# Kernel tuning notes

Hardware: AMD Instinct MI355X
Metric: run time of the kernel (lower is better)

Reference implementation:

```python
import jax, jax.numpy as jnp
import numpy as np

MOMENTUM = 0.1  # from init_kwargs


def setup_inputs() -> dict:
    key = jax.random.key(0)
    k1, k2 = jax.random.split(key)
    # [B, C, H, W] image batch
    x = jax.random.normal(k1, (32, 3, 512, 512), dtype=jnp.float32)
    # running amplitude buffer [C, H, W]; nonzero -> EMA branch is exercised
    running_amp = jax.random.uniform(k2, (3, 512, 512), dtype=jnp.float32)
    return {"x": x, "running_amp": running_amp}


def reference(x, running_amp):
    # FFT over spatial dims
    fft = jnp.fft.fft2(x, axes=(-2, -1))                     # [B,C,H,W] complex64
    amp = jnp.fft.fftshift(jnp.abs(fft), axes=(-2, -1))      # centered amplitude
    pha = jnp.angle(fft)                                     # phase

    # EMA update of running amplitude (batch-mean); if buffer is all-zero it is
    # initialized to the batch mean (mirrors the torch `sum == 0` branch).
    amp_mean = jnp.mean(amp, axis=0)                         # [C,H,W]
    new_amp = jnp.where(
        jnp.sum(running_amp) == 0,
        amp_mean,
        (1.0 - MOMENTUM) * running_amp + MOMENTUM * amp_mean,
    )

    # substitute amplitude with the (updated) running amplitude, keep phase
    amp_sub = jnp.fft.ifftshift(new_amp, axes=(-2, -1))      # [C,H,W]
    out = jnp.real(jnp.fft.ifft2(amp_sub * jnp.exp(1j * pha), axes=(-2, -1)))
    return out.astype(x.dtype)
```

## Files before the change

### kernel.cpp

```cpp
#include <hip/hip_runtime.h>
#include <math.h>

#define NB 32
#define NC 3
#define HH 512
#define WW 512
#define W2 272


__device__ __forceinline__ int swz(int i){ int h=(i>>6)&7; return i ^ (h<<3) ^ h; }
__device__ __forceinline__ int rev9(int k){ return ((k&7)<<6) | (k&56) | (k>>6); }

__device__ __forceinline__ float sin2pi(float x){
#if __has_builtin(__builtin_amdgcn_sinf)
  return __builtin_amdgcn_sinf(x);
#else
  return __sinf(6.28318530717958647692f*x);
#endif
}
__device__ __forceinline__ float cos2pi(float x){
#if __has_builtin(__builtin_amdgcn_cosf)
  return __builtin_amdgcn_cosf(x);
#else
  return __cosf(6.28318530717958647692f*x);
#endif
}

template<int S>
__device__ __forceinline__ void dft8(float* xr, float* xi){
  const float r2 = 0.70710678118654752f;
  float tr[4], ti[4], mr[4], mi[4];
#pragma unroll
  for(int n=0;n<4;n++){
    tr[n]=xr[n]+xr[n+4]; ti[n]=xi[n]+xi[n+4];
    mr[n]=xr[n]-xr[n+4]; mi[n]=xi[n]-xi[n+4];
  }
  float or_[4], oi_[4];
  or_[0]=mr[0];               oi_[0]=mi[0];
  or_[1]=r2*(mr[1]-S*mi[1]);  oi_[1]=r2*(mi[1]+S*mr[1]);
  or_[2]=-S*mi[2];            oi_[2]= S*mr[2];
  or_[3]=-r2*(mr[3]+S*mi[3]); oi_[3]= r2*(S*mr[3]-mi[3]);
  float s0r=tr[0]+tr[2], s0i=ti[0]+ti[2];
  float s1r=tr[1]+tr[3], s1i=ti[1]+ti[3];
  float d0r=tr[0]-tr[2], d0i=ti[0]-ti[2];
  float d1r=tr[1]-tr[3], d1i=ti[1]-ti[3];
  xr[0]=s0r+s1r;   xi[0]=s0i+s1i;
  xr[4]=s0r-s1r;   xi[4]=s0i-s1i;
  xr[2]=d0r-S*d1i; xi[2]=d0i+S*d1r;
  xr[6]=d0r+S*d1i; xi[6]=d0i-S*d1r;
  float p0r=or_[0]+or_[2], p0i=oi_[0]+oi_[2];
  float p1r=or_[1]+or_[3], p1i=oi_[1]+oi_[3];
  float e0r=or_[0]-or_[2], e0i=oi_[0]-oi_[2];
  float e1r=or_[1]-or_[3], e1i=oi_[1]-oi_[3];
  xr[1]=p0r+p1r;   xi[1]=p0i+p1i;
  xr[5]=p0r-p1r;   xi[5]=p0i-p1i;
  xr[3]=e0r-S*e1i; xi[3]=e0i+S*e1r;
  xr[7]=e0r+S*e1i; xi[7]=e0i-S*e1r;
}

template<int S>
__device__ __forceinline__ void twid(float* xr, float* xi, int n, float invM){
  float f = (float)n * invM;
  float c1 = cos2pi(f), s1 = (float)S * sin2pi(f);
  float cr=c1, ci=s1;
#pragma unroll
  for(int q=1;q<8;q++){
    float a=xr[q], b=xi[q];
    xr[q]=a*cr-b*ci; xi[q]=a*ci+b*cr;
    float nr=cr*c1-ci*s1, ni=cr*s1+ci*c1;
    cr=nr; ci=ni;
  }
}

__global__ __launch_bounds__(256) void k_row_rfft(const float* __restrict__ x, float2* __restrict__ Fh,
                                                  int c0, unsigned long long fh_cs){
  __shared__ float lre[4][512];
  __shared__ float lim[4][512];
  const int wv = threadIdx.x>>6, t = threadIdx.x&63;
  const int pr = blockIdx.x*4 + wv;
  const int b = pr>>8, r2 = pr&255;
  const int cc = blockIdx.y, c = c0 + cc;
  const float* sa = x + (size_t)b*(NC*HH*WW) + (size_t)c*HH*WW + (size_t)(2*r2)*WW;
  const float* sb = sa + WW;
  float xr[8], xi[8];
#pragma unroll
  for(int i=0;i<8;i++){ xr[i]=sa[t+64*i]; xi[i]=sb[t+64*i]; }
  dft8<-1>(xr,xi);
  twid<-1>(xr,xi,t,1.0f/512.0f);
#pragma unroll
  for(int q=0;q<8;q++){ int p=swz(t+64*q); lre[wv][p]=xr[q]; lim[wv][p]=xi[q]; }
  __syncthreads();
  const int beta=t>>3, n1=t&7, base1=64*beta+n1;
#pragma unroll
  for(int i=0;i<8;i++){ int p=swz(base1+8*i); xr[i]=lre[wv][p]; xi[i]=lim[wv][p]; }
  dft8<-1>(xr,xi);
  twid<-1>(xr,xi,n1,1.0f/64.0f);
#pragma unroll
  for(int q=0;q<8;q++){ int p=swz(base1+8*q); lre[wv][p]=xr[q]; lim[wv][p]=xi[q]; }
  __syncthreads();
#pragma unroll
  for(int i=0;i<8;i++){ int p=swz(8*t+i); xr[i]=lre[wv][p]; xi[i]=lim[wv][p]; }
  dft8<-1>(xr,xi);
  __syncthreads();
#pragma unroll
  for(int i=0;i<8;i++){ int nat = 64*i + 8*(t&7) + (t>>3); lre[wv][nat]=xr[i]; lim[wv][nat]=xi[i]; }
  __syncthreads();
  float2* Fa = Fh + (size_t)cc*fh_cs + (size_t)(b*HH + 2*r2)*W2;
  float2* Fb = Fa + W2;
#pragma unroll
  for(int j=0;j<5;j++){
    int w = t + 64*j;
    if(w<=256){
      int m = (512-w)&511;
      float pr_=lre[wv][w], pi_=lim[wv][w], qr=lre[wv][m], qi=lim[wv][m];
      Fa[w]=make_float2(0.5f*(pr_+qr), 0.5f*(pi_-qi));
      Fb[w]=make_float2(0.5f*(pi_+qi), 0.5f*(qr-pr_));
    }
  }
}

__global__ __launch_bounds__(512) void k_col_fft(float2* __restrict__ Fh, unsigned long long fh_cs){
  __shared__ float sre[512*17];
  __shared__ float sim[512*17];
  const int b    = blockIdx.x/17;
  const int tile = blockIdx.x - b*17;
  const int w0   = tile*16;
  float2* base = Fh + (size_t)blockIdx.y*fh_cs + (size_t)b*HH*W2 + w0;
  const int c = threadIdx.x&15, w = threadIdx.x>>4;
#pragma unroll
  for(int k=0;k<16;k++){
    int f = threadIdx.x + 512*k;
    int r = f>>4, col = f&15;
    float2 v = base[(size_t)r*W2 + col];
    sre[r*17+col]=v.x; sim[r*17+col]=v.y;
  }
  __syncthreads();
#pragma unroll
  for(int jj=0;jj<2;jj++){
    int n = jj*32 + w;
    float xr[8], xi[8];
#pragma unroll
    for(int i=0;i<8;i++){ int e=n+64*i; xr[i]=sre[e*17+c]; xi[i]=sim[e*17+c]; }
    dft8<-1>(xr,xi);
    twid<-1>(xr,xi,n,1.0f/512.0f);
#pragma unroll
    for(int q=0;q<8;q++){ int e=n+64*q; sre[e*17+c]=xr[q]; sim[e*17+c]=xi[q]; }
  }
  __syncthreads();
#pragma unroll
  for(int jj=0;jj<2;jj++){
    int m = jj*32 + w;
    int bb = m>>3, nn = m&7, bs = 64*bb+nn;
    float xr[8], xi[8];
#pragma unroll
    for(int i=0;i<8;i++){ int e=bs+8*i; xr[i]=sre[e*17+c]; xi[i]=sim[e*17+c]; }
    dft8<-1>(xr,xi);
    twid<-1>(xr,xi,nn,1.0f/64.0f);
#pragma unroll
    for(int q=0;q<8;q++){ int e=bs+8*q; sre[e*17+c]=xr[q]; sim[e*17+c]=xi[q]; }
  }
  __syncthreads();
#pragma unroll
  for(int jj=0;jj<2;jj++){
    int m = jj*32+w;
    float xr[8], xi[8];
#pragma unroll
    for(int i=0;i<8;i++){ int e=8*m+i; xr[i]=sre[e*17+c]; xi[i]=sim[e*17+c]; }
    dft8<-1>(xr,xi);
#pragma unroll
    for(int q=0;q<8;q++){ int e=8*m+q; sre[e*17+c]=xr[q]; sim[e*17+c]=xi[q]; }
  }
  __syncthreads();
#pragma unroll
  for(int k=0;k<16;k++){
    int f=threadIdx.x+512*k;
    int r=f>>4, col=f&15;
    if(w0+col<=256)
      base[(size_t)r*W2+col]=make_float2(sre[r*17+col], sim[r*17+col]);
  }
}

__global__ __launch_bounds__(256) void k_rsum(const float* __restrict__ ra, float* __restrict__ out, int n){
  float s=0.f;
  for(int i=blockIdx.x*256+threadIdx.x; i<n; i+=gridDim.x*256) s+=ra[i];
#pragma unroll
  for(int off=32;off>=1;off>>=1) s += __shfl_down(s, off, 64);
  if((threadIdx.x&63)==0) atomicAdd(out, s);
}

__global__ __launch_bounds__(256) void k_amp(const float2* __restrict__ Fh, unsigned long long fh_cs,
                                             const float* __restrict__ ra, const float* __restrict__ rsum,
                                             float* __restrict__ A, unsigned long long a_cs, int c0){
  int f = blockIdx.x*256 + threadIdx.x;
  int p = f/W2, w = f - p*W2;
  if(w>256) return;
  const int cc = blockIdx.y, c = c0 + cc;
  const float2* Fc = Fh + (size_t)cc*fh_cs;
  const float* rac = ra + (size_t)c*HH*WW;
  float s=0.f;
#pragma unroll 8
  for(int b=0;b<NB;b++){
    float2 v = Fc[((size_t)b*HH + p)*W2 + w];
    s += sqrtf(v.x*v.x+v.y*v.y);
  }
  float mean = s*(1.0f/32.0f);
  int h = rev9(p);
  int hs =(h+256)&511, ws =(w+256)&511;
  int hs2=(256-h)&511, ws2=(256-w)&511;
  float a_ = (rsum[0]==0.0f) ? mean
           : 0.45f*(rac[hs*WW+ws] + rac[hs2*WW+ws2]) + 0.1f*mean;
  A[(size_t)cc*a_cs + f]=a_;
}

__global__ __launch_bounds__(512) void k_col_ifft(float2* __restrict__ Fh, unsigned long long fh_cs,
                                                  const float* __restrict__ A, unsigned long long a_cs){
  __shared__ float sre[512*17];
  __shared__ float sim[512*17];
  const int b    = blockIdx.x/17;
  const int tile = blockIdx.x - b*17;
  const int w0   = tile*16;
  float2* base = Fh + (size_t)blockIdx.y*fh_cs + (size_t)b*HH*W2 + w0;
  const float* Aa = A + (size_t)blockIdx.y*a_cs + w0;
  const int c = threadIdx.x&15, w = threadIdx.x>>4;
  const float invN2 = 1.0f/262144.0f;
#pragma unroll
  for(int k=0;k<16;k++){
    int f=threadIdx.x+512*k;
    int r=f>>4, col=f&15;
    float2 v = base[(size_t)r*W2+col];
    float amp = Aa[(size_t)r*W2+col];
    float mag = sqrtf(v.x*v.x + v.y*v.y);
    float fr, fi;
    if(mag > 0.f){ float sc = amp*invN2/mag; fr=v.x*sc; fi=v.y*sc; }
    else         { fr = amp*invN2; fi=0.f; }
    sre[r*17+col]=fr; sim[r*17+col]=fi;
  }
  __syncthreads();
#pragma unroll
  for(int jj=0;jj<2;jj++){
    int m = jj*32+w;
    float xr[8], xi[8];
#pragma unroll
    for(int q=0;q<8;q++){ int e=8*m+q; xr[q]=sre[e*17+c]; xi[q]=sim[e*17+c]; }
    dft8<1>(xr,xi);
#pragma unroll
    for(int i=0;i<8;i++){ int e=8*m+i; sre[e*17+c]=xr[i]; sim[e*17+c]=xi[i]; }
  }
  __syncthreads();
#pragma unroll
  for(int jj=0;jj<2;jj++){
    int m = jj*32 + w;
    int bb = m>>3, nn = m&7, bs = 64*bb+nn;
    float xr[8], xi[8];
#pragma unroll
    for(int q=0;q<8;q++){ int e=bs+8*q; xr[q]=sre[e*17+c]; xi[q]=sim[e*17+c]; }
    twid<1>(xr,xi,nn,1.0f/64.0f);
    dft8<1>(xr,xi);
#pragma unroll
    for(int i=0;i<8;i++){ int e=bs+8*i; sre[e*17+c]=xr[i]; sim[e*17+c]=xi[i]; }
  }
  __syncthreads();
#pragma unroll
  for(int jj=0;jj<2;jj++){
    int n = jj*32+w;
    float xr[8], xi[8];
#pragma unroll
    for(int q=0;q<8;q++){ int e=n+64*q; xr[q]=sre[e*17+c]; xi[q]=sim[e*17+c]; }
    twid<1>(xr,xi,n,1.0f/512.0f);
    dft8<1>(xr,xi);
#pragma unroll
    for(int i=0;i<8;i++){ int e=n+64*i; sre[e*17+c]=xr[i]; sim[e*17+c]=xi[i]; }
  }
  __syncthreads();
#pragma unroll
  for(int k=0;k<16;k++){
    int f=threadIdx.x+512*k;
    int r=f>>4, col=f&15;
    if(w0+col<=256)
      base[(size_t)r*W2+col]=make_float2(sre[r*17+col], sim[r*17+col]);
  }
}

__global__ __launch_bounds__(256) void k_row_irfft(const float2* __restrict__ Fh, unsigned long long fh_cs,
                                                   float* __restrict__ out, int c0){
  __shared__ float gAr[4][264], gAi[4][264], gBr[4][264], gBi[4][264];
  __shared__ float lre[4][512], lim[4][512];
  const int wv=threadIdx.x>>6, t=threadIdx.x&63;
  const int pr = blockIdx.x*4+wv;
  const int b = pr>>8, r2 = pr&255;
  const int cc = blockIdx.y, c = c0 + cc;
  const float2* Rp = Fh + (size_t)cc*fh_cs + (size_t)(b*HH + 2*r2)*W2;
  const float2* Rq = Rp + W2;
#pragma unroll
  for(int j=0;j<5;j++){
    int w = t + 64*j;
    if(w<=256){
      float2 v = Rp[w]; gAr[wv][w]=v.x; gAi[wv][w]=v.y;
      float2 u = Rq[w]; gBr[wv][w]=u.x; gBi[wv][w]=u.y;
    }
  }
  __syncthreads();
  float xr[8], xi[8];
#pragma unroll
  for(int i=0;i<8;i++){
    int w = rev9(8*t+i);
    float zr, zi;
    if(w<=256){ zr = gAr[wv][w]-gBi[wv][w]; zi = gAi[wv][w]+gBr[wv][w]; }
    else{
      int m = 512-w;
      zr = gAr[wv][m]+gBi[wv][m]; zi = gBr[wv][m]-gAi[wv][m];
    }
    xr[i]=zr; xi[i]=zi;
  }
  dft8<1>(xr,xi);
#pragma unroll
  for(int i=0;i<8;i++){ int pp=swz(8*t+i); lre[wv][pp]=xr[i]; lim[wv][pp]=xi[i]; }
  __syncthreads();
  const int beta=t>>3, n1=t&7, base1=64*beta+n1;
#pragma unroll
  for(int qq=0;qq<8;qq++){ int pp=swz(base1+8*qq); xr[qq]=lre[wv][pp]; xi[qq]=lim[wv][pp]; }
  twid<1>(xr,xi,n1,1.0f/64.0f);
  dft8<1>(xr,xi);
#pragma unroll
  for(int i=0;i<8;i++){ int pp=swz(base1+8*i); lre[wv][pp]=xr[i]; lim[wv][pp]=xi[i]; }
  __syncthreads();
#pragma unroll
  for(int qq=0;qq<8;qq++){ int pp=swz(t+64*qq); xr[qq]=lre[wv][pp]; xi[qq]=lim[wv][pp]; }
  twid<1>(xr,xi,t,1.0f/512.0f);
  dft8<1>(xr,xi);
  float* oa = out + (size_t)b*(NC*HH*WW) + (size_t)c*HH*WW + (size_t)(2*r2)*WW;
  float* ob = oa + WW;
#pragma unroll
  for(int i=0;i<8;i++){ oa[t+64*i]=xr[i]; ob[t+64*i]=xi[i]; }
}

extern "C" void kernel_launch(void* const* d_in, const int* in_sizes, int n_in,
                              void* d_out, int out_size, void* d_ws, size_t ws_size,
                              hipStream_t stream) {
  const float* x  = (const float*)d_in[0];
  const float* ra = (const float*)d_in[1];
  float* out = (float*)d_out;

  const unsigned long long fh_cs = (unsigned long long)NB*HH*W2;
  const unsigned long long a_cs  = (unsigned long long)HH*W2;
  const size_t fb1 = (size_t)fh_cs*sizeof(float2);
  const size_t ab1 = (size_t)a_cs*sizeof(float);
  const size_t need3 = 3*fb1 + 3*ab1 + 64;
  const size_t need1 = fb1 + ab1 + 64;

  if (ws_size >= need3) {
    float2* Fh   = (float2*)d_ws;
    float*  A    = (float*)((char*)d_ws + 3*fb1);
    float*  rsum = (float*)((char*)A + 3*ab1);
    hipMemsetAsync(rsum, 0, sizeof(float), stream);
    k_rsum<<<768,256,0,stream>>>(ra, rsum, NC*HH*WW);
    k_row_rfft <<<dim3(NB*256/4,3), 256, 0, stream>>>(x, Fh, 0, fh_cs);
    k_col_fft  <<<dim3(NB*17,3),    512, 0, stream>>>(Fh, fh_cs);
    k_amp      <<<dim3(HH*W2/256,3),256, 0, stream>>>(Fh, fh_cs, ra, rsum, A, a_cs, 0);
    k_col_ifft <<<dim3(NB*17,3),    512, 0, stream>>>(Fh, fh_cs, A, a_cs);
    k_row_irfft<<<dim3(NB*256/4,3), 256, 0, stream>>>(Fh, fh_cs, out, 0);
  } else if (ws_size >= need1) {
    float2* Fh   = (float2*)d_ws;
    float*  A    = (float*)((char*)d_ws + fb1);
    float*  rsum = (float*)((char*)A + ab1);
    hipMemsetAsync(rsum, 0, sizeof(float), stream);
    k_rsum<<<768,256,0,stream>>>(ra, rsum, NC*HH*WW);
    for(int c=0;c<NC;c++){
      k_row_rfft <<<dim3(NB*256/4,1), 256, 0, stream>>>(x, Fh, c, 0ULL);
      k_col_fft  <<<dim3(NB*17,1),    512, 0, stream>>>(Fh, 0ULL);
      k_amp      <<<dim3(HH*W2/256,1),256, 0, stream>>>(Fh, 0ULL, ra, rsum, A, 0ULL, c);
      k_col_ifft <<<dim3(NB*17,1),    512, 0, stream>>>(Fh, 0ULL, A, 0ULL);
      k_row_irfft<<<dim3(NB*256/4,1), 256, 0, stream>>>(Fh, 0ULL, out, c);
    }
  }
}
```

Baseline: 241.6 us.

## Fuse amplitude batch-sum into column FFT and load/store columns directly from global

The column FFT and inverse FFT kernels now read the first stage and write the last stage directly from and to global memory, skipping the shared-memory staging passes and their barriers. The column FFT also accumulates per-frequency magnitudes into a zeroed buffer with atomicAdd, so the amplitude kernel no longer rereads the whole spectrum across the batch and only finalizes the mean and EMA. The per-channel fallback path for small workspaces is removed, and the inverse uses rsqrt instead of sqrt and a divide. The trade-offs are strided, less coalesced global accesses and 32-way atomic contention per output element.

```diff
diff --git a/kernel.cpp b/kernel.cpp
--- a/kernel.cpp
+++ b/kernel.cpp
@@ -73,14 +73,14 @@
 }
 
 __global__ __launch_bounds__(256) void k_row_rfft(const float* __restrict__ x, float2* __restrict__ Fh,
-                                                  int c0, unsigned long long fh_cs){
+                                                  unsigned long long fh_cs){
   __shared__ float lre[4][512];
   __shared__ float lim[4][512];
   const int wv = threadIdx.x>>6, t = threadIdx.x&63;
   const int pr = blockIdx.x*4 + wv;
   const int b = pr>>8, r2 = pr&255;
-  const int cc = blockIdx.y, c = c0 + cc;
-  const float* sa = x + (size_t)b*(NC*HH*WW) + (size_t)c*HH*WW + (size_t)(2*r2)*WW;
+  const int cc = blockIdx.y;
+  const float* sa = x + (size_t)b*(NC*HH*WW) + (size_t)cc*HH*WW + (size_t)(2*r2)*WW;
   const float* sb = sa + WW;
   float xr[8], xi[8];
 #pragma unroll
@@ -119,28 +119,23 @@
   }
 }
 
-__global__ __launch_bounds__(512) void k_col_fft(float2* __restrict__ Fh, unsigned long long fh_cs){
+__global__ __launch_bounds__(512) void k_col_fft(float2* __restrict__ Fh, unsigned long long fh_cs,
+                                                 float* __restrict__ Asum, unsigned long long a_cs){
   __shared__ float sre[512*17];
   __shared__ float sim[512*17];
   const int b    = blockIdx.x/17;
   const int tile = blockIdx.x - b*17;
   const int w0   = tile*16;
-  float2* base = Fh + (size_t)blockIdx.y*fh_cs + (size_t)b*HH*W2 + w0;
+  const int cc   = blockIdx.y;
+  float2* base = Fh + (size_t)cc*fh_cs + (size_t)b*HH*W2 + w0;
+  float*  As   = Asum + (size_t)cc*a_cs + w0;
   const int c = threadIdx.x&15, w = threadIdx.x>>4;
 #pragma unroll
-  for(int k=0;k<16;k++){
-    int f = threadIdx.x + 512*k;
-    int r = f>>4, col = f&15;
-    float2 v = base[(size_t)r*W2 + col];
-    sre[r*17+col]=v.x; sim[r*17+col]=v.y;
-  }
-  __syncthreads();
-#pragma unroll
   for(int jj=0;jj<2;jj++){
     int n = jj*32 + w;
     float xr[8], xi[8];
 #pragma unroll
-    for(int i=0;i<8;i++){ int e=n+64*i; xr[i]=sre[e*17+c]; xi[i]=sim[e*17+c]; }
+    for(int i=0;i<8;i++){ float2 v = base[(size_t)(n+64*i)*W2 + c]; xr[i]=v.x; xi[i]=v.y; }
     dft8<-1>(xr,xi);
     twid<-1>(xr,xi,n,1.0f/512.0f);
 #pragma unroll
@@ -167,16 +162,14 @@
 #pragma unroll
     for(int i=0;i<8;i++){ int e=8*m+i; xr[i]=sre[e*17+c]; xi[i]=sim[e*17+c]; }
     dft8<-1>(xr,xi);
-#pragma unroll
-    for(int q=0;q<8;q++){ int e=8*m+q; sre[e*17+c]=xr[q]; sim[e*17+c]=xi[q]; }
-  }
-  __syncthreads();
-#pragma unroll
-  for(int k=0;k<16;k++){
-    int f=threadIdx.x+512*k;
-    int r=f>>4, col=f&15;
-    if(w0+col<=256)
-      base[(size_t)r*W2+col]=make_float2(sre[r*17+col], sim[r*17+col]);
+    if(w0+c<=256){
+#pragma unroll
+      for(int q=0;q<8;q++){
+        int p=8*m+q;
+        base[(size_t)p*W2+c]=make_float2(xr[q],xi[q]);
+        atomicAdd(&As[(size_t)p*W2+c], sqrtf(xr[q]*xr[q]+xi[q]*xi[q]));
+      }
+    }
   }
 }
 
@@ -188,22 +181,16 @@
   if((threadIdx.x&63)==0) atomicAdd(out, s);
 }
 
-__global__ __launch_bounds__(256) void k_amp(const float2* __restrict__ Fh, unsigned long long fh_cs,
-                                             const float* __restrict__ ra, const float* __restrict__ rsum,
-                                             float* __restrict__ A, unsigned long long a_cs, int c0){
+__global__ __launch_bounds__(256) void k_amp_fin(const float* __restrict__ Asum, unsigned long long a_cs,
+                                                 const float* __restrict__ ra, const float* __restrict__ rsum,
+                                                 float* __restrict__ A){
   int f = blockIdx.x*256 + threadIdx.x;
+  if(f >= HH*W2) return;
   int p = f/W2, w = f - p*W2;
   if(w>256) return;
-  const int cc = blockIdx.y, c = c0 + cc;
-  const float2* Fc = Fh + (size_t)cc*fh_cs;
-  const float* rac = ra + (size_t)c*HH*WW;
-  float s=0.f;
-#pragma unroll 8
-  for(int b=0;b<NB;b++){
-    float2 v = Fc[((size_t)b*HH + p)*W2 + w];
-    s += sqrtf(v.x*v.x+v.y*v.y);
-  }
-  float mean = s*(1.0f/32.0f);
+  const int cc = blockIdx.y;
+  float mean = Asum[(size_t)cc*a_cs + f]*(1.0f/32.0f);
+  const float* rac = ra + (size_t)cc*HH*WW;
   int h = rev9(p);
   int hs =(h+256)&511, ws =(w+256)&511;
   int hs2=(256-h)&511, ws2=(256-w)&511;
@@ -219,29 +206,25 @@
   const int b    = blockIdx.x/17;
   const int tile = blockIdx.x - b*17;
   const int w0   = tile*16;
-  float2* base = Fh + (size_t)blockIdx.y*fh_cs + (size_t)b*HH*W2 + w0;
-  const float* Aa = A + (size_t)blockIdx.y*a_cs + w0;
+  const int cc   = blockIdx.y;
+  float2* base = Fh + (size_t)cc*fh_cs + (size_t)b*HH*W2 + w0;
+  const float* Aa = A + (size_t)cc*a_cs + w0;
   const int c = threadIdx.x&15, w = threadIdx.x>>4;
   const float invN2 = 1.0f/262144.0f;
 #pragma unroll
-  for(int k=0;k<16;k++){
-    int f=threadIdx.x+512*k;
-    int r=f>>4, col=f&15;
-    float2 v = base[(size_t)r*W2+col];
-    float amp = Aa[(size_t)r*W2+col];
-    float mag = sqrtf(v.x*v.x + v.y*v.y);
-    float fr, fi;
-    if(mag > 0.f){ float sc = amp*invN2/mag; fr=v.x*sc; fi=v.y*sc; }
-    else         { fr = amp*invN2; fi=0.f; }
-    sre[r*17+col]=fr; sim[r*17+col]=fi;
-  }
-  __syncthreads();
-#pragma unroll
   for(int jj=0;jj<2;jj++){
     int m = jj*32+w;
     float xr[8], xi[8];
 #pragma unroll
-    for(int q=0;q<8;q++){ int e=8*m+q; xr[q]=sre[e*17+c]; xi[q]=sim[e*17+c]; }
+    for(int q=0;q<8;q++){
+      int p=8*m+q;
+      float2 v = base[(size_t)p*W2+c];
+      float amp = Aa[(size_t)p*W2+c];
+      float m2 = v.x*v.x + v.y*v.y;
+      float sc = amp*invN2*__frsqrt_rn(m2);
+      if(m2 > 0.f){ xr[q]=v.x*sc; xi[q]=v.y*sc; }
+      else        { xr[q]=amp*invN2; xi[q]=0.f; }
+    }
     dft8<1>(xr,xi);
 #pragma unroll
     for(int i=0;i<8;i++){ int e=8*m+i; sre[e*17+c]=xr[i]; sim[e*17+c]=xi[i]; }
@@ -268,27 +251,21 @@
     for(int q=0;q<8;q++){ int e=n+64*q; xr[q]=sre[e*17+c]; xi[q]=sim[e*17+c]; }
     twid<1>(xr,xi,n,1.0f/512.0f);
     dft8<1>(xr,xi);
-#pragma unroll
-    for(int i=0;i<8;i++){ int e=n+64*i; sre[e*17+c]=xr[i]; sim[e*17+c]=xi[i]; }
-  }
-  __syncthreads();
-#pragma unroll
-  for(int k=0;k<16;k++){
-    int f=threadIdx.x+512*k;
-    int r=f>>4, col=f&15;
-    if(w0+col<=256)
-      base[(size_t)r*W2+col]=make_float2(sre[r*17+col], sim[r*17+col]);
+    if(w0+c<=256){
+#pragma unroll
+      for(int i=0;i<8;i++){ base[(size_t)(n+64*i)*W2+c]=make_float2(xr[i],xi[i]); }
+    }
   }
 }
 
 __global__ __launch_bounds__(256) void k_row_irfft(const float2* __restrict__ Fh, unsigned long long fh_cs,
-                                                   float* __restrict__ out, int c0){
+                                                   float* __restrict__ out){
   __shared__ float gAr[4][264], gAi[4][264], gBr[4][264], gBi[4][264];
   __shared__ float lre[4][512], lim[4][512];
   const int wv=threadIdx.x>>6, t=threadIdx.x&63;
   const int pr = blockIdx.x*4+wv;
   const int b = pr>>8, r2 = pr&255;
-  const int cc = blockIdx.y, c = c0 + cc;
+  const int cc = blockIdx.y;
   const float2* Rp = Fh + (size_t)cc*fh_cs + (size_t)(b*HH + 2*r2)*W2;
   const float2* Rq = Rp + W2;
 #pragma unroll
@@ -328,7 +305,7 @@
   for(int qq=0;qq<8;qq++){ int pp=swz(t+64*qq); xr[qq]=lre[wv][pp]; xi[qq]=lim[wv][pp]; }
   twid<1>(xr,xi,t,1.0f/512.0f);
   dft8<1>(xr,xi);
-  float* oa = out + (size_t)b*(NC*HH*WW) + (size_t)c*HH*WW + (size_t)(2*r2)*WW;
+  float* oa = out + (size_t)b*(NC*HH*WW) + (size_t)cc*HH*WW + (size_t)(2*r2)*WW;
   float* ob = oa + WW;
 #pragma unroll
   for(int i=0;i<8;i++){ oa[t+64*i]=xr[i]; ob[t+64*i]=xi[i]; }
@@ -343,34 +320,22 @@
 
   const unsigned long long fh_cs = (unsigned long long)NB*HH*W2;
   const unsigned long long a_cs  = (unsigned long long)HH*W2;
-  const size_t fb1 = (size_t)fh_cs*sizeof(float2);
+  const size_t fb3 = (size_t)fh_cs*sizeof(float2)*3;
   const size_t ab1 = (size_t)a_cs*sizeof(float);
-  const size_t need3 = 3*fb1 + 3*ab1 + 64;
-  const size_t need1 = fb1 + ab1 + 64;
-
-  if (ws_size >= need3) {
-    float2* Fh   = (float2*)d_ws;
-    float*  A    = (float*)((char*)d_ws + 3*fb1);
-    float*  rsum = (float*)((char*)A + 3*ab1);
-    hipMemsetAsync(rsum, 0, sizeof(float), stream);
-    k_rsum<<<768,256,0,stream>>>(ra, rsum, NC*HH*WW);
-    k_row_rfft <<<dim3(NB*256/4,3), 256, 0, stream>>>(x, Fh, 0, fh_cs);
-    k_col_fft  <<<dim3(NB*17,3),    512, 0, stream>>>(Fh, fh_cs);
-    k_amp      <<<dim3(HH*W2/256,3),256, 0, stream>>>(Fh, fh_cs, ra, rsum, A, a_cs, 0);
-    k_col_ifft <<<dim3(NB*17,3),    512, 0, stream>>>(Fh, fh_cs, A, a_cs);
-    k_row_irfft<<<dim3(NB*256/4,3), 256, 0, stream>>>(Fh, fh_cs, out, 0);
-  } else if (ws_size >= need1) {
-    float2* Fh   = (float2*)d_ws;
-    float*  A    = (float*)((char*)d_ws + fb1);
-    float*  rsum = (float*)((char*)A + ab1);
-    hipMemsetAsync(rsum, 0, sizeof(float), stream);
-    k_rsum<<<768,256,0,stream>>>(ra, rsum, NC*HH*WW);
-    for(int c=0;c<NC;c++){
-      k_row_rfft <<<dim3(NB*256/4,1), 256, 0, stream>>>(x, Fh, c, 0ULL);
-      k_col_fft  <<<dim3(NB*17,1),    512, 0, stream>>>(Fh, 0ULL);
-      k_amp      <<<dim3(HH*W2/256,1),256, 0, stream>>>(Fh, 0ULL, ra, rsum, A, 0ULL, c);
-      k_col_ifft <<<dim3(NB*17,1),    512, 0, stream>>>(Fh, 0ULL, A, 0ULL);
-      k_row_irfft<<<dim3(NB*256/4,1), 256, 0, stream>>>(Fh, 0ULL, out, c);
-    }
-  }
-}
+  const size_t need = fb3 + 3*ab1 + 64 + 3*ab1;
+  if (ws_size < need) return;
+
+  float2* Fh   = (float2*)d_ws;
+  float*  Asum = (float*)((char*)d_ws + fb3);
+  float*  rsum = (float*)((char*)Asum + 3*ab1);
+  float*  A    = (float*)((char*)rsum + 64);
+
+  hipMemsetAsync(Asum, 0, 3*ab1 + sizeof(float), stream);
+  k_rsum<<<768,256,0,stream>>>(ra, rsum, NC*HH*WW);
+
+  k_row_rfft <<<dim3(NB*256/4,3), 256, 0, stream>>>(x, Fh, fh_cs);
+  k_col_fft  <<<dim3(NB*17,3),    512, 0, stream>>>(Fh, fh_cs, Asum, a_cs);
+  k_amp_fin  <<<dim3((HH*W2+255)/256,3), 256, 0, stream>>>(Asum, a_cs, ra, rsum, A);
+  k_col_ifft <<<dim3(NB*17,3),    512, 0, stream>>>(Fh, fh_cs, A, a_cs);
+  k_row_irfft<<<dim3(NB*256/4,3), 256, 0, stream>>>(Fh, fh_cs, out);
+}
```

Result: faster. 228.9 us (-5.3%).
